# Optimization experiments

Hardware: AMD Instinct MI355X
Metric: run time of the kernel (lower is better)

## Reference

```python
import jax, jax.numpy as jnp
import numpy as np


def setup_inputs() -> dict:
    key = jax.random.key(0)
    ks = jax.random.split(key, 6)
    B, HW, CIN, COUT, K = 256, 64, 3, 128, 32
    inputs = jax.random.normal(ks[0], (B, HW, HW, CIN), jnp.float32)
    conv_w = jax.random.normal(ks[1], (3, 3, CIN, COUT), jnp.float32) * 0.1
    conv_b = jnp.zeros((COUT,), jnp.float32)
    match_w = jax.random.normal(ks[2], (COUT,), jnp.float32) * 0.1
    match_b = jnp.zeros((1,), jnp.float32)
    pat_w = jax.random.normal(ks[3], (32 * 32 * K, 1), jnp.float32) * 0.01
    pat_b = jnp.zeros((1,), jnp.float32)
    base_w = jax.random.normal(ks[4], (32 * 32 * COUT, 3), jnp.float32) * 0.01
    base_b = jnp.zeros((3,), jnp.float32)
    pattern_set_index = jax.random.randint(ks[5], (K,), 0, COUT, jnp.int32)
    return {
        "inputs": inputs, "conv_w": conv_w, "conv_b": conv_b,
        "match_w": match_w, "match_b": match_b,
        "pat_w": pat_w, "pat_b": pat_b,
        "base_w": base_w, "base_b": base_b,
        "pattern_set_index": pattern_set_index,
    }


def reference(inputs, conv_w, conv_b, match_w, match_b,
              pat_w, pat_b, base_w, base_b, pattern_set_index):
    B = inputs.shape[0]
    # feat_extract: conv3x3 stride 2 + relu -> feats0 [B,32,32,128]; GAP -> feats1 [B,128]
    feats0 = jax.nn.relu(
        jax.lax.conv_general_dilated(
            inputs, conv_w, window_strides=(2, 2), padding='SAME',
            dimension_numbers=('NHWC', 'HWIO', 'NHWC')) + conv_b)
    feats1 = feats0.mean(axis=(1, 2))  # [B,128]
    # pat_matcher: boolean per-sample match mask
    matches = (feats1 @ match_w + match_b[0]) > 0.0  # [B] bool
    # pat_pred on channel-subset features (tf.gather axis=3)
    sel = jnp.take(feats0, pattern_set_index, axis=3)  # [B,32,32,32]
    p = jax.nn.sigmoid(sel.reshape(B, -1) @ pat_w + pat_b)[:, 0]  # [B]
    # BinaryToCategorical(pattern_class=0, num_classes=3): [p, (1-p)/2, (1-p)/2]
    o = (1.0 - p) * 0.5
    cat = jnp.stack([p, o, o], axis=-1)  # [B,3]
    # base_pred on full features (used for matched-low and non-matched samples)
    base = jax.nn.softmax(feats0.reshape(B, -1) @ base_w + base_b, axis=-1)  # [B,3]
    # route: matched AND pat score >= 0.5 -> categorized pat pred, else base pred
    use_pat = matches & (p >= 0.5)
    return jnp.where(use_pat[:, None], cat, base)
```

## Files before the change

### kernel.cpp

```cpp
#include <hip/hip_runtime.h>
#include <math.h>

#define TPB 512

__global__ __launch_bounds__(256)
void prep_weights(const float* __restrict__ base_w,
                  const float* __restrict__ pat_w,
                  const int*   __restrict__ psi,
                  float4* __restrict__ wq)
{
    int idx = blockIdx.x * 256 + threadIdx.x;
    int hw = idx >> 7, c = idx & 127;
    const float* bp = base_w + (size_t)idx * 3;
    float b0 = bp[0], b1 = bp[1], b2 = bp[2];
    float pc = 0.f;
    const float* pr = pat_w + hw * 32;
    #pragma unroll
    for (int k = 0; k < 32; ++k)
        pc += (psi[k] == c) ? pr[k] : 0.f;
    wq[idx] = make_float4(b0, b1, b2, pc);
}

__global__ __launch_bounds__(TPB, 8)
void pattern_branch_kernel(const float* __restrict__ in,
                           const float* __restrict__ conv_w,
                           const float* __restrict__ conv_b,
                           const float* __restrict__ match_w,
                           const float4* __restrict__ wq,
                           float* __restrict__ part)
{
    constexpr int ROWF4 = 50;
    __shared__ float4 xlds4[17 * ROWF4];
    __shared__ float  red[8][5];

    const int bx  = blockIdx.x;
    const int qh  = bx >> 8;
    const int b   = bx & 255;
    const int tid = threadIdx.x;

    for (int s = tid; s < 17 * ROWF4; s += TPB) xlds4[s] = make_float4(0.f, 0.f, 0.f, 0.f);
    __syncthreads();
    const float4* inp4 = (const float4*)(in + (size_t)b * 12288);
    for (int s = tid; s < 17 * 48; s += TPB) {
        int r  = s / 48;
        int qq = s - r * 48;
        int ih = 16 * qh + r;
        if (ih < 64) xlds4[r * ROWF4 + qq] = inp4[ih * 48 + qq];
    }
    __syncthreads();

    const int c  = tid & 127;
    const int sg = tid >> 7;
    float w[27];
    #pragma unroll
    for (int k = 0; k < 27; ++k) w[k] = conv_w[k * 128 + c];
    const float bias = conv_b[c];
    const float mw   = match_w[c];

    float s_match = 0.f, sb0 = 0.f, sb1 = 0.f, sb2 = 0.f, s_pat = 0.f;

    for (int it = 0; it < 16; ++it) {
        int slot   = it * 4 + sg;
        int oh_loc = slot >> 3;
        int q      = slot & 7;
        float acc[4] = { bias, bias, bias, bias };

        #pragma unroll
        for (int kh = 0; kh < 3; ++kh) {
            const float4* rp = &xlds4[(2 * oh_loc + kh) * ROWF4 + 6 * q];
            {
                float4 t0 = rp[0], t1 = rp[1], t2 = rp[2], t3 = rp[3];
                float x[16] = { t0.x,t0.y,t0.z,t0.w, t1.x,t1.y,t1.z,t1.w,
                                t2.x,t2.y,t2.z,t2.w, t3.x,t3.y,t3.z,t3.w };
                #pragma unroll
                for (int t9 = 0; t9 < 9; ++t9) {
                    float wk = w[kh * 9 + t9];
                    acc[0] = fmaf(x[t9],     wk, acc[0]);
                    acc[1] = fmaf(x[6 + t9], wk, acc[1]);
                }
            }
            {
                float4 t0 = rp[3], t1 = rp[4], t2 = rp[5], t3 = rp[6];
                float x[16] = { t0.x,t0.y,t0.z,t0.w, t1.x,t1.y,t1.z,t1.w,
                                t2.x,t2.y,t2.z,t2.w, t3.x,t3.y,t3.z,t3.w };
                #pragma unroll
                for (int t9 = 0; t9 < 9; ++t9) {
                    float wk = w[kh * 9 + t9];
                    acc[2] = fmaf(x[t9],     wk, acc[2]);
                    acc[3] = fmaf(x[6 + t9], wk, acc[3]);
                }
            }
        }
        int hwbase = (8 * qh + oh_loc) * 32 + 4 * q;
        #pragma unroll
        for (int v = 0; v < 4; ++v) {
            float fv = fmaxf(acc[v], 0.f);
            float4 wv = wq[(size_t)(hwbase + v) * 128 + c];
            s_match = fmaf(mw, fv, s_match);
            sb0   = fmaf(fv, wv.x, sb0);
            sb1   = fmaf(fv, wv.y, sb1);
            sb2   = fmaf(fv, wv.z, sb2);
            s_pat = fmaf(fv, wv.w, s_pat);
        }
    }

    float vals[5] = { s_match, sb0, sb1, sb2, s_pat };
    #pragma unroll
    for (int off = 32; off > 0; off >>= 1)
        #pragma unroll
        for (int v = 0; v < 5; ++v)
            vals[v] += __shfl_down(vals[v], off, 64);
    int wv = tid >> 6, lane = tid & 63;
    if (lane == 0) {
        #pragma unroll
        for (int v = 0; v < 5; ++v) red[wv][v] = vals[v];
    }
    __syncthreads();
    if (tid == 0) {
        #pragma unroll
        for (int v = 0; v < 5; ++v) {
            float t = 0.f;
            for (int wj = 0; wj < 8; ++wj) t += red[wj][v];
            part[(qh * 5 + v) * 256 + b] = t;
        }
    }
}

__global__ __launch_bounds__(256)
void finalize_kernel(const float* __restrict__ part,
                     const float* __restrict__ match_b,
                     const float* __restrict__ pat_b,
                     const float* __restrict__ base_b,
                     float* __restrict__ out)
{
    int b = threadIdx.x;
    float t[5] = { 0.f, 0.f, 0.f, 0.f, 0.f };
    #pragma unroll
    for (int j = 0; j < 4; ++j)
        #pragma unroll
        for (int v = 0; v < 5; ++v)
            t[v] += part[(j * 5 + v) * 256 + b];
    float score = t[0] * (1.f / 1024.f) + match_b[0];
    float p = 1.f / (1.f + expf(-(t[4] + pat_b[0])));
    float l0 = t[1] + base_b[0], l1 = t[2] + base_b[1], l2 = t[3] + base_b[2];
    float m = fmaxf(l0, fmaxf(l1, l2));
    float e0 = expf(l0 - m), e1 = expf(l1 - m), e2 = expf(l2 - m);
    float inv = 1.f / (e0 + e1 + e2);
    bool use_pat = (score > 0.f) && (p >= 0.5f);
    float o0, o1, o2;
    if (use_pat) { o0 = p; o1 = 0.5f * (1.f - p); o2 = o1; }
    else         { o0 = e0 * inv; o1 = e1 * inv; o2 = e2 * inv; }
    out[b * 3 + 0] = o0;
    out[b * 3 + 1] = o1;
    out[b * 3 + 2] = o2;
}

extern "C" void kernel_launch(void* const* d_in, const int* in_sizes, int n_in,
                              void* d_out, int out_size, void* d_ws, size_t ws_size,
                              hipStream_t stream) {
    const float* in      = (const float*)d_in[0];
    const float* conv_w  = (const float*)d_in[1];
    const float* conv_b  = (const float*)d_in[2];
    const float* match_w = (const float*)d_in[3];
    const float* match_b = (const float*)d_in[4];
    const float* pat_w   = (const float*)d_in[5];
    const float* pat_b   = (const float*)d_in[6];
    const float* base_w  = (const float*)d_in[7];
    const float* base_b  = (const float*)d_in[8];
    const int*   psi     = (const int*)d_in[9];
    float* out = (float*)d_out;

    float4* wq   = (float4*)d_ws;
    float*  part = (float*)((char*)d_ws + (size_t)131072 * 16);

    prep_weights<<<512, 256, 0, stream>>>(base_w, pat_w, psi, wq);

    int B = in_sizes[0] / (64 * 64 * 3);
    pattern_branch_kernel<<<4 * B, TPB, 0, stream>>>(
        in, conv_w, conv_b, match_w, wq, part);

    finalize_kernel<<<1, 256, 0, stream>>>(part, match_b, pat_b, base_b, out);
}
```

Before: 118.4 us.

## Remap conv kernel to sample-per-lane with channel-uniform weights and spatial slices

Restructures the main kernel so each block covers a spatial slice (one output row quarter) for 64 samples, with lanes indexing samples and waves iterating channels. Conv weights, bias and match weights are pre-transposed into a wave-uniform table, so they can be read as scalar loads and the per-pixel head weights are shared across lanes. The head weights are read once per slice instead of once per sample, and the partial sums are reduced in the finalize kernel over 128 slices. The cost is strided, uncoalesced input gathers into shared memory, a larger partial buffer, and a heavier finalize step. The grid size is now hardcoded to 512 blocks, which assumes B=256.

```diff
diff --git a/kernel.cpp b/kernel.cpp
--- a/kernel.cpp
+++ b/kernel.cpp
@@ -7,7 +7,11 @@
 void prep_weights(const float* __restrict__ base_w,
                   const float* __restrict__ pat_w,
                   const int*   __restrict__ psi,
-                  float4* __restrict__ wq)
+                  const float* __restrict__ conv_w,
+                  const float* __restrict__ conv_b,
+                  const float* __restrict__ match_w,
+                  float4* __restrict__ wq,
+                  float*  __restrict__ cwT)
 {
     int idx = blockIdx.x * 256 + threadIdx.x;
     int hw = idx >> 7, c = idx & 127;
@@ -19,110 +23,95 @@
     for (int k = 0; k < 32; ++k)
         pc += (psi[k] == c) ? pr[k] : 0.f;
     wq[idx] = make_float4(b0, b1, b2, pc);
+
+    if (idx < 4096) {
+        int cc = idx >> 5, k = idx & 31;
+        float v = 0.f;
+        if (k < 27)       v = conv_w[k * 128 + cc];
+        else if (k == 27) v = conv_b[cc];
+        else if (k == 28) v = match_w[cc];
+        cwT[idx] = v;
+    }
 }
 
 __global__ __launch_bounds__(TPB, 8)
 void pattern_branch_kernel(const float* __restrict__ in,
-                           const float* __restrict__ conv_w,
-                           const float* __restrict__ conv_b,
-                           const float* __restrict__ match_w,
-                           const float4* __restrict__ wq,
+                           const float* __restrict__ cwT,
+                           const float* __restrict__ wq,
                            float* __restrict__ part)
 {
-    constexpr int ROWF4 = 50;
-    __shared__ float4 xlds4[17 * ROWF4];
-    __shared__ float  red[8][5];
+    __shared__ float xs[3 * 52 * 64];
+    __shared__ float red[8][5][64];
 
-    const int bx  = blockIdx.x;
-    const int qh  = bx >> 8;
-    const int b   = bx & 255;
-    const int tid = threadIdx.x;
+    const int bx    = blockIdx.x;
+    const int sg    = bx & 3;
+    const int slice = bx >> 2;
+    const int oh    = slice >> 2;
+    const int owq   = slice & 3;
+    const int tid   = threadIdx.x;
 
-    for (int s = tid; s < 17 * ROWF4; s += TPB) xlds4[s] = make_float4(0.f, 0.f, 0.f, 0.f);
+    for (int i = tid; i < 3 * 52 * 64; i += TPB) xs[i] = 0.f;
     __syncthreads();
-    const float4* inp4 = (const float4*)(in + (size_t)b * 12288);
-    for (int s = tid; s < 17 * 48; s += TPB) {
-        int r  = s / 48;
-        int qq = s - r * 48;
-        int ih = 16 * qh + r;
-        if (ih < 64) xlds4[r * ROWF4 + qq] = inp4[ih * 48 + qq];
+
+    {
+        const int s = tid & 63;
+        const float4* src = (const float4*)in + (size_t)(64 * sg + s) * 3072;
+        const int nq = (owq < 3) ? 13 : 12;
+        for (int idx = tid >> 6; idx < 39; idx += 8) {
+            int r = idx / 13, q = idx - r * 13;
+            int ih = 2 * oh + r;
+            if (ih < 64 && q < nq) {
+                float4 v = src[ih * 48 + 12 * owq + q];
+                int f = 4 * q;
+                xs[(r * 52 + f)     * 64 + s] = v.x;
+                xs[(r * 52 + f + 1) * 64 + s] = v.y;
+                xs[(r * 52 + f + 2) * 64 + s] = v.z;
+                xs[(r * 52 + f + 3) * 64 + s] = v.w;
+            }
+        }
     }
     __syncthreads();
 
-    const int c  = tid & 127;
-    const int sg = tid >> 7;
-    float w[27];
-    #pragma unroll
-    for (int k = 0; k < 27; ++k) w[k] = conv_w[k * 128 + c];
-    const float bias = conv_b[c];
-    const float mw   = match_w[c];
+    const int s  = tid & 63;
+    const int wv = __builtin_amdgcn_readfirstlane(tid >> 6);
+    float sm = 0.f, s0 = 0.f, s1 = 0.f, s2 = 0.f, sp = 0.f;
+    const int hwbase = oh * 32 + 8 * owq;
 
-    float s_match = 0.f, sb0 = 0.f, sb1 = 0.f, sb2 = 0.f, s_pat = 0.f;
+    for (int px = 0; px < 8; ++px) {
+        float x[27];
+        #pragma unroll
+        for (int kh = 0; kh < 3; ++kh)
+            #pragma unroll
+            for (int t = 0; t < 9; ++t)
+                x[kh * 9 + t] = xs[(kh * 52 + 6 * px + t) * 64 + s];
 
-    for (int it = 0; it < 16; ++it) {
-        int slot   = it * 4 + sg;
-        int oh_loc = slot >> 3;
-        int q      = slot & 7;
-        float acc[4] = { bias, bias, bias, bias };
-
-        #pragma unroll
-        for (int kh = 0; kh < 3; ++kh) {
-            const float4* rp = &xlds4[(2 * oh_loc + kh) * ROWF4 + 6 * q];
-            {
-                float4 t0 = rp[0], t1 = rp[1], t2 = rp[2], t3 = rp[3];
-                float x[16] = { t0.x,t0.y,t0.z,t0.w, t1.x,t1.y,t1.z,t1.w,
-                                t2.x,t2.y,t2.z,t2.w, t3.x,t3.y,t3.z,t3.w };
-                #pragma unroll
-                for (int t9 = 0; t9 < 9; ++t9) {
-                    float wk = w[kh * 9 + t9];
-                    acc[0] = fmaf(x[t9],     wk, acc[0]);
-                    acc[1] = fmaf(x[6 + t9], wk, acc[1]);
-                }
-            }
-            {
-                float4 t0 = rp[3], t1 = rp[4], t2 = rp[5], t3 = rp[6];
-                float x[16] = { t0.x,t0.y,t0.z,t0.w, t1.x,t1.y,t1.z,t1.w,
-                                t2.x,t2.y,t2.z,t2.w, t3.x,t3.y,t3.z,t3.w };
-                #pragma unroll
-                for (int t9 = 0; t9 < 9; ++t9) {
-                    float wk = w[kh * 9 + t9];
-                    acc[2] = fmaf(x[t9],     wk, acc[2]);
-                    acc[3] = fmaf(x[6 + t9], wk, acc[3]);
-                }
-            }
-        }
-        int hwbase = (8 * qh + oh_loc) * 32 + 4 * q;
-        #pragma unroll
-        for (int v = 0; v < 4; ++v) {
-            float fv = fmaxf(acc[v], 0.f);
-            float4 wv = wq[(size_t)(hwbase + v) * 128 + c];
-            s_match = fmaf(mw, fv, s_match);
-            sb0   = fmaf(fv, wv.x, sb0);
-            sb1   = fmaf(fv, wv.y, sb1);
-            sb2   = fmaf(fv, wv.z, sb2);
-            s_pat = fmaf(fv, wv.w, s_pat);
+        const float* wqp = wq + (size_t)(hwbase + px) * 512;
+        #pragma unroll 2
+        for (int j = 0; j < 16; ++j) {
+            int c = wv * 16 + j;
+            const float* cw = cwT + c * 32;
+            float acc = cw[27];
+            #pragma unroll
+            for (int k = 0; k < 27; ++k) acc = fmaf(x[k], cw[k], acc);
+            float f = fmaxf(acc, 0.f);
+            const float* q4 = wqp + c * 4;
+            sm = fmaf(cw[28], f, sm);
+            s0 = fmaf(f, q4[0], s0);
+            s1 = fmaf(f, q4[1], s1);
+            s2 = fmaf(f, q4[2], s2);
+            sp = fmaf(f, q4[3], sp);
         }
     }
 
-    float vals[5] = { s_match, sb0, sb1, sb2, s_pat };
-    #pragma unroll
-    for (int off = 32; off > 0; off >>= 1)
+    red[wv][0][s] = sm; red[wv][1][s] = s0; red[wv][2][s] = s1;
+    red[wv][3][s] = s2; red[wv][4][s] = sp;
+    __syncthreads();
+    if (tid < 320) {
+        int v = tid >> 6, ss = tid & 63;
+        float a = 0.f;
         #pragma unroll
-        for (int v = 0; v < 5; ++v)
-            vals[v] += __shfl_down(vals[v], off, 64);
-    int wv = tid >> 6, lane = tid & 63;
-    if (lane == 0) {
-        #pragma unroll
-        for (int v = 0; v < 5; ++v) red[wv][v] = vals[v];
-    }
-    __syncthreads();
-    if (tid == 0) {
-        #pragma unroll
-        for (int v = 0; v < 5; ++v) {
-            float t = 0.f;
-            for (int wj = 0; wj < 8; ++wj) t += red[wj][v];
-            part[(qh * 5 + v) * 256 + b] = t;
-        }
+        for (int w2 = 0; w2 < 8; ++w2) a += red[w2][v][ss];
+        part[((size_t)v * 256 + 64 * sg + ss) * 128 + slice] = a;
     }
 }
 
@@ -134,12 +123,18 @@
                      float* __restrict__ out)
 {
     int b = threadIdx.x;
-    float t[5] = { 0.f, 0.f, 0.f, 0.f, 0.f };
+    float t[5];
     #pragma unroll
-    for (int j = 0; j < 4; ++j)
+    for (int v = 0; v < 5; ++v) {
+        const float4* p4 = (const float4*)(part + ((size_t)v * 256 + b) * 128);
+        float a = 0.f;
         #pragma unroll
-        for (int v = 0; v < 5; ++v)
-            t[v] += part[(j * 5 + v) * 256 + b];
+        for (int i = 0; i < 32; ++i) {
+            float4 u = p4[i];
+            a += (u.x + u.y) + (u.z + u.w);
+        }
+        t[v] = a;
+    }
     float score = t[0] * (1.f / 1024.f) + match_b[0];
     float p = 1.f / (1.f + expf(-(t[4] + pat_b[0])));
     float l0 = t[1] + base_b[0], l1 = t[2] + base_b[1], l2 = t[3] + base_b[2];
@@ -170,14 +165,15 @@
     const int*   psi     = (const int*)d_in[9];
     float* out = (float*)d_out;
 
-    float4* wq   = (float4*)d_ws;
-    float*  part = (float*)((char*)d_ws + (size_t)131072 * 16);
+    char* ws = (char*)d_ws;
+    float4* wq   = (float4*)ws;
+    float*  cwT  = (float*)(ws + (size_t)131072 * 16);
+    float*  part = (float*)(ws + (size_t)131072 * 16 + 16384);
 
-    prep_weights<<<512, 256, 0, stream>>>(base_w, pat_w, psi, wq);
+    prep_weights<<<512, 256, 0, stream>>>(base_w, pat_w, psi,
+                                          conv_w, conv_b, match_w, wq, cwT);
 
-    int B = in_sizes[0] / (64 * 64 * 3);
-    pattern_branch_kernel<<<4 * B, TPB, 0, stream>>>(
-        in, conv_w, conv_b, match_w, wq, part);
+    pattern_branch_kernel<<<512, TPB, 0, stream>>>(in, cwT, (const float*)wq, part);
 
     finalize_kernel<<<1, 256, 0, stream>>>(part, match_b, pat_b, base_b, out);
 }
```

Result: slower. 148.0 us (+25.0%).

## Interleave routed weights per 4-pixel group and remap thread slots to contiguous rows

Applied to the files above, without the earlier changes.

Prep now writes the fused base/pattern weight float4s so that the four consecutive output pixels a thread handles sit next to each other per channel. Each thread now sweeps contiguous slots, and its weight pointer advances by a fixed stride instead of being recomputed per pixel. The convolution taps are written out explicitly with asm register pins, and the match sum combines four pixels before one FMA. The occupancy hint in launch bounds drops from 8 to 6, which gives more registers per thread but may lower latency hiding.

```diff
diff --git a/kernel.cpp b/kernel.cpp
--- a/kernel.cpp
+++ b/kernel.cpp
@@ -7,7 +7,7 @@
 void prep_weights(const float* __restrict__ base_w,
                   const float* __restrict__ pat_w,
                   const int*   __restrict__ psi,
-                  float4* __restrict__ wq)
+                  float4* __restrict__ wq2)
 {
     int idx = blockIdx.x * 256 + threadIdx.x;
     int hw = idx >> 7, c = idx & 127;
@@ -18,15 +18,15 @@
     #pragma unroll
     for (int k = 0; k < 32; ++k)
         pc += (psi[k] == c) ? pr[k] : 0.f;
-    wq[idx] = make_float4(b0, b1, b2, pc);
+    wq2[(size_t)((hw >> 2) * 128 + c) * 4 + (hw & 3)] = make_float4(b0, b1, b2, pc);
 }
 
-__global__ __launch_bounds__(TPB, 8)
+__global__ __launch_bounds__(TPB, 6)
 void pattern_branch_kernel(const float* __restrict__ in,
                            const float* __restrict__ conv_w,
                            const float* __restrict__ conv_b,
                            const float* __restrict__ match_w,
-                           const float4* __restrict__ wq,
+                           const float4* __restrict__ wq2,
                            float* __restrict__ part)
 {
     constexpr int ROWF4 = 50;
@@ -54,57 +54,71 @@
     float w[27];
     #pragma unroll
     for (int k = 0; k < 27; ++k) w[k] = conv_w[k * 128 + c];
-    const float bias = conv_b[c];
-    const float mw   = match_w[c];
+    float bias = conv_b[c];
+    float mw   = match_w[c];
+    #pragma unroll
+    for (int k = 0; k < 27; ++k) asm volatile("" : "+v"(w[k]));
+    asm volatile("" : "+v"(bias), "+v"(mw));
 
-    float s_match = 0.f, sb0 = 0.f, sb1 = 0.f, sb2 = 0.f, s_pat = 0.f;
+    float sm = 0.f, s0 = 0.f, s1 = 0.f, s2 = 0.f, sp = 0.f;
+
+    const float4* wqp = wq2 + (size_t)((8 * qh + 2 * sg) * 8) * 512 / 4 * 4;
+    wqp = wq2 + (size_t)((8 * qh + 2 * sg) * 8 * 128 + c) * 4;
 
     for (int it = 0; it < 16; ++it) {
-        int slot   = it * 4 + sg;
-        int oh_loc = slot >> 3;
-        int q      = slot & 7;
-        float acc[4] = { bias, bias, bias, bias };
+        const int oh_loc = 2 * sg + (it >> 3);
+        const int q      = it & 7;
 
+        float acc0 = bias, acc1 = bias, acc2 = bias, acc3 = bias;
         #pragma unroll
         for (int kh = 0; kh < 3; ++kh) {
-            const float4* rp = &xlds4[(2 * oh_loc + kh) * ROWF4 + 6 * q];
+            const float4* rp = &xlds4[(4 * sg + 2 * (it >> 3) + kh) * ROWF4 + 6 * q];
+            const float* wk = &w[kh * 9];
             {
                 float4 t0 = rp[0], t1 = rp[1], t2 = rp[2], t3 = rp[3];
-                float x[16] = { t0.x,t0.y,t0.z,t0.w, t1.x,t1.y,t1.z,t1.w,
-                                t2.x,t2.y,t2.z,t2.w, t3.x,t3.y,t3.z,t3.w };
-                #pragma unroll
-                for (int t9 = 0; t9 < 9; ++t9) {
-                    float wk = w[kh * 9 + t9];
-                    acc[0] = fmaf(x[t9],     wk, acc[0]);
-                    acc[1] = fmaf(x[6 + t9], wk, acc[1]);
-                }
+                acc0 = fmaf(t0.x, wk[0], acc0); acc0 = fmaf(t0.y, wk[1], acc0);
+                acc0 = fmaf(t0.z, wk[2], acc0); acc0 = fmaf(t0.w, wk[3], acc0);
+                acc0 = fmaf(t1.x, wk[4], acc0); acc0 = fmaf(t1.y, wk[5], acc0);
+                acc0 = fmaf(t1.z, wk[6], acc0); acc0 = fmaf(t1.w, wk[7], acc0);
+                acc0 = fmaf(t2.x, wk[8], acc0);
+                acc1 = fmaf(t1.z, wk[0], acc1); acc1 = fmaf(t1.w, wk[1], acc1);
+                acc1 = fmaf(t2.x, wk[2], acc1); acc1 = fmaf(t2.y, wk[3], acc1);
+                acc1 = fmaf(t2.z, wk[4], acc1); acc1 = fmaf(t2.w, wk[5], acc1);
+                acc1 = fmaf(t3.x, wk[6], acc1); acc1 = fmaf(t3.y, wk[7], acc1);
+                acc1 = fmaf(t3.z, wk[8], acc1);
             }
             {
-                float4 t0 = rp[3], t1 = rp[4], t2 = rp[5], t3 = rp[6];
-                float x[16] = { t0.x,t0.y,t0.z,t0.w, t1.x,t1.y,t1.z,t1.w,
-                                t2.x,t2.y,t2.z,t2.w, t3.x,t3.y,t3.z,t3.w };
-                #pragma unroll
-                for (int t9 = 0; t9 < 9; ++t9) {
-                    float wk = w[kh * 9 + t9];
-                    acc[2] = fmaf(x[t9],     wk, acc[2]);
-                    acc[3] = fmaf(x[6 + t9], wk, acc[3]);
-                }
+                float4 t3 = rp[3], t4 = rp[4], t5 = rp[5], t6 = rp[6];
+                acc2 = fmaf(t3.x, wk[0], acc2); acc2 = fmaf(t3.y, wk[1], acc2);
+                acc2 = fmaf(t3.z, wk[2], acc2); acc2 = fmaf(t3.w, wk[3], acc2);
+                acc2 = fmaf(t4.x, wk[4], acc2); acc2 = fmaf(t4.y, wk[5], acc2);
+                acc2 = fmaf(t4.z, wk[6], acc2); acc2 = fmaf(t4.w, wk[7], acc2);
+                acc2 = fmaf(t5.x, wk[8], acc2);
+                acc3 = fmaf(t4.z, wk[0], acc3); acc3 = fmaf(t4.w, wk[1], acc3);
+                acc3 = fmaf(t5.x, wk[2], acc3); acc3 = fmaf(t5.y, wk[3], acc3);
+                acc3 = fmaf(t5.z, wk[4], acc3); acc3 = fmaf(t5.w, wk[5], acc3);
+                acc3 = fmaf(t6.x, wk[6], acc3); acc3 = fmaf(t6.y, wk[7], acc3);
+                acc3 = fmaf(t6.z, wk[8], acc3);
             }
         }
-        int hwbase = (8 * qh + oh_loc) * 32 + 4 * q;
-        #pragma unroll
-        for (int v = 0; v < 4; ++v) {
-            float fv = fmaxf(acc[v], 0.f);
-            float4 wv = wq[(size_t)(hwbase + v) * 128 + c];
-            s_match = fmaf(mw, fv, s_match);
-            sb0   = fmaf(fv, wv.x, sb0);
-            sb1   = fmaf(fv, wv.y, sb1);
-            sb2   = fmaf(fv, wv.z, sb2);
-            s_pat = fmaf(fv, wv.w, s_pat);
-        }
+        float4 wv0 = wqp[0], wv1 = wqp[1], wv2 = wqp[2], wv3 = wqp[3];
+        wqp += 512;
+
+        float f0 = fmaxf(acc0, 0.f), f1 = fmaxf(acc1, 0.f);
+        float f2 = fmaxf(acc2, 0.f), f3 = fmaxf(acc3, 0.f);
+        sm = fmaf(mw, (f0 + f1) + (f2 + f3), sm);
+        s0 = fmaf(f0, wv0.x, s0); s1 = fmaf(f0, wv0.y, s1);
+        s2 = fmaf(f0, wv0.z, s2); sp = fmaf(f0, wv0.w, sp);
+        s0 = fmaf(f1, wv1.x, s0); s1 = fmaf(f1, wv1.y, s1);
+        s2 = fmaf(f1, wv1.z, s2); sp = fmaf(f1, wv1.w, sp);
+        s0 = fmaf(f2, wv2.x, s0); s1 = fmaf(f2, wv2.y, s1);
+        s2 = fmaf(f2, wv2.z, s2); sp = fmaf(f2, wv2.w, sp);
+        s0 = fmaf(f3, wv3.x, s0); s1 = fmaf(f3, wv3.y, s1);
+        s2 = fmaf(f3, wv3.z, s2); sp = fmaf(f3, wv3.w, sp);
+        (void)oh_loc; (void)q;
     }
 
-    float vals[5] = { s_match, sb0, sb1, sb2, s_pat };
+    float vals[5] = { sm, s0, s1, s2, sp };
     #pragma unroll
     for (int off = 32; off > 0; off >>= 1)
         #pragma unroll
@@ -170,14 +184,14 @@
     const int*   psi     = (const int*)d_in[9];
     float* out = (float*)d_out;
 
-    float4* wq   = (float4*)d_ws;
+    float4* wq2  = (float4*)d_ws;
     float*  part = (float*)((char*)d_ws + (size_t)131072 * 16);
 
-    prep_weights<<<512, 256, 0, stream>>>(base_w, pat_w, psi, wq);
+    prep_weights<<<512, 256, 0, stream>>>(base_w, pat_w, psi, wq2);
 
     int B = in_sizes[0] / (64 * 64 * 3);
     pattern_branch_kernel<<<4 * B, TPB, 0, stream>>>(
-        in, conv_w, conv_b, match_w, wq, part);
+        in, conv_w, conv_b, match_w, wq2, part);
 
     finalize_kernel<<<1, 256, 0, stream>>>(part, match_b, pat_b, base_b, out);
 }
```

New measurement: 123.5 us. +4.4%, slower.
